# Kernel tuning notes

Measured on AMD Instinct MI355X. Metric: run time of the kernel, lower is better.

The kernel has to match this reference:

```python
import jax, jax.numpy as jnp
import numpy as np

HEAD_DIM = 128
N_HEADS = 32
N_KV_HEADS = 8
EPS = 1e-6
ROPE_THETA = 1e6
NEG_INF = -1e9


def _rms_norm(x, w):
    # per-head RMSNorm over last dim (head_dim), fp32 math like Qwen3RMSNorm
    xf = x.astype(jnp.float32)
    var = jnp.mean(xf * xf, axis=-1, keepdims=True)
    return (w * (xf * jax.lax.rsqrt(var + EPS))).astype(x.dtype)


def _rope_cos_sin(position_ids, dtype):
    # default rope: inv_freq = theta^(-2i/d), emb = cat(freqs, freqs)
    inv_freq = 1.0 / (ROPE_THETA ** (jnp.arange(0, HEAD_DIM, 2, dtype=jnp.float32) / HEAD_DIM))
    freqs = position_ids.astype(jnp.float32)[:, :, None] * inv_freq[None, None, :]  # [B,S,hd/2]
    emb = jnp.concatenate([freqs, freqs], axis=-1)  # [B,S,hd]
    return jnp.cos(emb).astype(dtype), jnp.sin(emb).astype(dtype)


def _rotate_half(x):
    x1, x2 = jnp.split(x, 2, axis=-1)
    return jnp.concatenate([-x2, x1], axis=-1)


def setup_inputs() -> dict:
    key = jax.random.key(0)
    ks = jax.random.split(key, 6)
    B, S, H = 1, 2048, 4096
    return {
        "hidden_states": jax.random.normal(ks[0], (B, S, H), jnp.float32),
        "position_ids": jnp.broadcast_to(jnp.arange(S, dtype=jnp.int32)[None, :], (B, S)),
        "Wq": jax.random.normal(ks[1], (N_HEADS * HEAD_DIM, H), jnp.float32) * 0.02,
        "Wk": jax.random.normal(ks[2], (N_KV_HEADS * HEAD_DIM, H), jnp.float32) * 0.02,
        "Wv": jax.random.normal(ks[3], (N_KV_HEADS * HEAD_DIM, H), jnp.float32) * 0.02,
        "Wo": jax.random.normal(ks[4], (H, N_HEADS * HEAD_DIM), jnp.float32) * 0.02,
        "q_norm_w": jnp.ones((HEAD_DIM,), jnp.float32),
        "k_norm_w": jnp.ones((HEAD_DIM,), jnp.float32),
    }


def reference(hidden_states, position_ids, Wq, Wk, Wv, Wo, q_norm_w, k_norm_w):
    B, S, H = hidden_states.shape
    scaling = HEAD_DIM ** -0.5
    n_rep = N_HEADS // N_KV_HEADS

    # projections (torch Linear: y = x @ W.T), reshape to [B, heads, S, hd]
    q = jnp.einsum('bsh,dh->bsd', hidden_states, Wq).reshape(B, S, N_HEADS, HEAD_DIM)
    k = jnp.einsum('bsh,dh->bsd', hidden_states, Wk).reshape(B, S, N_KV_HEADS, HEAD_DIM)
    v = jnp.einsum('bsh,dh->bsd', hidden_states, Wv).reshape(B, S, N_KV_HEADS, HEAD_DIM)

    q = _rms_norm(q, q_norm_w).transpose(0, 2, 1, 3)  # [B,nH,S,hd]
    k = _rms_norm(k, k_norm_w).transpose(0, 2, 1, 3)  # [B,nKV,S,hd]
    v = v.transpose(0, 2, 1, 3)

    cos, sin = _rope_cos_sin(position_ids, hidden_states.dtype)
    cos = cos[:, None, :, :]  # unsqueeze head dim
    sin = sin[:, None, :, :]
    q = q * cos + _rotate_half(q) * sin
    k = k * cos + _rotate_half(k) * sin

    # GQA repeat_kv
    k = jnp.repeat(k, n_rep, axis=1)
    v = jnp.repeat(v, n_rep, axis=1)

    scores = jnp.einsum('bhqd,bhkd->bhqk', q, k) * scaling
    causal = jnp.where(
        jnp.arange(S)[:, None] >= jnp.arange(S)[None, :], 0.0, NEG_INF
    ).astype(scores.dtype)
    scores = scores + causal[None, None, :, :]
    attn = jax.nn.softmax(scores.astype(jnp.float32), axis=-1).astype(q.dtype)

    out = jnp.einsum('bhqk,bhkd->bhqd', attn, v)
    out = out.transpose(0, 2, 1, 3).reshape(B, S, N_HEADS * HEAD_DIM)
    return jnp.einsum('bsd,hd->bsh', out, Wo)
```

## Files before the change

kernel.cpp:

```cpp
#include <hip/hip_runtime.h>
#include <hip/hip_bf16.h>

typedef unsigned short u16;
typedef __bf16 bf16x8 __attribute__((ext_vector_type(8)));
typedef u16 u16x4 __attribute__((ext_vector_type(4)));
typedef u16 u16x8 __attribute__((ext_vector_type(8)));
typedef float f32x4 __attribute__((ext_vector_type(4)));

#define S_LEN  2048
#define HID    4096
#define NHEADS 32
#define NKV    8
#define HD     128
#define QDIM   (NHEADS*HD)
#define KVDIM  (NKV*HD)
#define NT     (S_LEN/64)

__device__ __forceinline__ u16 f2bf(float f) {
  unsigned u = __float_as_uint(f);
  u += 0x7fff + ((u >> 16) & 1);
  return (u16)(u >> 16);
}
__device__ __forceinline__ void lds_load16(const u16* g, u16* l) {
  __builtin_amdgcn_global_load_lds(
      (__attribute__((address_space(1))) void*)(g),
      (__attribute__((address_space(3))) void*)(l), 16, 0, 0);
}

__global__ __launch_bounds__(256) void f2b4(
    const float* __restrict__ s0, u16* __restrict__ d0, long n0,
    const float* __restrict__ s1, u16* __restrict__ d1, long n1,
    const float* __restrict__ s2, u16* __restrict__ d2, long n2,
    const float* __restrict__ s3, u16* __restrict__ d3, long n3)
{
  const float* s; u16* d; long n; int b0, nb;
  const int b = blockIdx.x;
  if (b < 1024)      { s=s0; d=d0; n=n0; b0=0;    nb=1024; }
  else if (b < 3072) { s=s1; d=d1; n=n1; b0=1024; nb=2048; }
  else if (b < 3584) { s=s2; d=d2; n=n2; b0=3072; nb=512;  }
  else               { s=s3; d=d3; n=n3; b0=3584; nb=512;  }
  long i = (long)(b - b0)*256 + threadIdx.x;
  const long stride = (long)nb*256;
  for (; i < n; i += stride) {
    f32x4 a = ((const f32x4*)s)[i*2];
    f32x4 c = ((const f32x4*)s)[i*2 + 1];
    u16x8 o;
    #pragma unroll
    for (int j = 0; j < 4; ++j) { o[j] = f2bf(a[j]); o[4+j] = f2bf(c[j]); }
    ((u16x8*)d)[i] = o;
  }
}

__global__ __launch_bounds__(256) void f2b(
    const float* __restrict__ in, u16* __restrict__ out, long n8)
{
  long i = (long)blockIdx.x * blockDim.x + threadIdx.x;
  const long stride = (long)gridDim.x * blockDim.x;
  for (; i < n8; i += stride) {
    f32x4 a = ((const f32x4*)in)[i*2];
    f32x4 b = ((const f32x4*)in)[i*2 + 1];
    u16x8 o;
    #pragma unroll
    for (int j = 0; j < 4; ++j) { o[j] = f2bf(a[j]); o[4+j] = f2bf(b[j]); }
    ((u16x8*)out)[i] = o;
  }
}

template<int CMODE>
__global__ __launch_bounds__(512, 2) void gemm8(
    const u16* __restrict__ A, const u16* __restrict__ B,
    void* __restrict__ Cq, void* __restrict__ Ck, void* __restrict__ Cv,
    int M, int N, int K)
{
  __shared__ u16 lds[65536];
  const int tid  = threadIdx.x;
  const int lane = tid & 63;
  const int w    = tid >> 6;
  const int wr   = w >> 2, wc = w & 3;
  const int l16  = lane & 15, lhi = lane >> 4;
  const long arow0 = (long)blockIdx.y * 256;
  const long brow0 = (long)blockIdx.x * 256;
  const int ntiles = K >> 6;

  const u16* Ag[2]; const u16* Bg[2];
  #pragma unroll
  for (int r = 0; r < 2; ++r) {
    const int p  = r*4096 + w*512 + lane*8;
    const int lr = p >> 6;
    const int cu = (p & 63) ^ ((lr & 7) << 3);
    Ag[r] = A + (arow0 + (lr >> 6)*128 + (lr & 63))*(long)K + cu;
    Bg[r] = B + (brow0 + (lr >> 5)*64  + (lr & 31))*(long)K + cu;
  }
  u16* const dstA = lds + w*512;
  u16* const dstB = lds + 32768 + w*512;

  auto stageA = [&](int s, int kt) {
    const long so = (long)(kt*64) + (long)(s*64)*K;
    u16* d = dstA + (((kt & 1)*2 + s) << 13);
    lds_load16(Ag[0] + so, d);
    lds_load16(Ag[1] + so, d + 4096);
  };
  auto stageB = [&](int s, int kt) {
    const long so = (long)(kt*64) + (long)(s*32)*K;
    u16* d = dstB + (((kt & 1)*2 + s) << 13);
    lds_load16(Bg[0] + so, d);
    lds_load16(Bg[1] + so, d + 4096);
  };

  const int xr = (l16 & 7) << 3;
  int offA[4][2], offB[2][2];
  #pragma unroll
  for (int m2 = 0; m2 < 4; ++m2)
    #pragma unroll
    for (int ks = 0; ks < 2; ++ks)
      offA[m2][ks] = (wr*64 + m2*16 + l16)*64 + ((ks*32 + lhi*8) ^ xr);
  #pragma unroll
  for (int n2 = 0; n2 < 2; ++n2)
    #pragma unroll
    for (int ks = 0; ks < 2; ++ks)
      offB[n2][ks] = (wc*32 + n2*16 + l16)*64 + ((ks*32 + lhi*8) ^ xr);

  f32x4 acc[8][4] = {};

  stageA(0, 0); stageB(0, 0); stageB(1, 0); stageA(1, 0);
  stageA(0, 1); stageB(0, 1); stageB(1, 1);
  asm volatile("s_waitcnt vmcnt(6)" ::: "memory");
  __builtin_amdgcn_s_barrier();

  #pragma unroll 2
  for (int t = 0; t < ntiles; ++t) {
    const int Ab = (t & 1) << 14;
    const int Bb = 32768 + ((t & 1) << 14);
    bf16x8 af[4][2], bf[2][2], af2[4][2], bf2[2][2];

    #pragma unroll
    for (int m2 = 0; m2 < 4; ++m2)
      #pragma unroll
      for (int ks = 0; ks < 2; ++ks)
        af[m2][ks] = *(const bf16x8*)(lds + Ab + offA[m2][ks]);
    #pragma unroll
    for (int n2 = 0; n2 < 2; ++n2)
      #pragma unroll
      for (int ks = 0; ks < 2; ++ks)
        bf[n2][ks] = *(const bf16x8*)(lds + Bb + offB[n2][ks]);
    if (t + 1 < ntiles) stageA(1, t + 1);
    __builtin_amdgcn_s_barrier();
    asm volatile("s_waitcnt lgkmcnt(0)" ::: "memory");
    __builtin_amdgcn_s_setprio(1);
    #pragma unroll
    for (int m2 = 0; m2 < 4; ++m2)
      #pragma unroll
      for (int n2 = 0; n2 < 2; ++n2)
        #pragma unroll
        for (int ks = 0; ks < 2; ++ks)
          acc[m2][n2] = __builtin_amdgcn_mfma_f32_16x16x32_bf16(
              af[m2][ks], bf[n2][ks], acc[m2][n2], 0, 0, 0);
    __builtin_amdgcn_s_setprio(0);
    __builtin_amdgcn_s_barrier();

    #pragma unroll
    for (int n2 = 0; n2 < 2; ++n2)
      #pragma unroll
      for (int ks = 0; ks < 2; ++ks)
        bf2[n2][ks] = *(const bf16x8*)(lds + Bb + 8192 + offB[n2][ks]);
    if (t + 2 < ntiles) stageA(0, t + 2);
    __builtin_amdgcn_s_barrier();
    asm volatile("s_waitcnt lgkmcnt(0)" ::: "memory");
    __builtin_amdgcn_s_setprio(1);
    #pragma unroll
    for (int m2 = 0; m2 < 4; ++m2)
      #pragma unroll
      for (int n2 = 0; n2 < 2; ++n2)
        #pragma unroll
        for (int ks = 0; ks < 2; ++ks)
          acc[m2][2+n2] = __builtin_amdgcn_mfma_f32_16x16x32_bf16(
              af[m2][ks], bf2[n2][ks], acc[m2][2+n2], 0, 0, 0);
    __builtin_amdgcn_s_setprio(0);
    __builtin_amdgcn_s_barrier();

    #pragma unroll
    for (int m2 = 0; m2 < 4; ++m2)
      #pragma unroll
      for (int ks = 0; ks < 2; ++ks)
        af2[m2][ks] = *(const bf16x8*)(lds + Ab + 8192 + offA[m2][ks]);
    if (t + 2 < ntiles) stageB(0, t + 2);
    __builtin_amdgcn_s_barrier();
    asm volatile("s_waitcnt lgkmcnt(0)" ::: "memory");
    __builtin_amdgcn_s_setprio(1);
    #pragma unroll
    for (int m2 = 0; m2 < 4; ++m2)
      #pragma unroll
      for (int n2 = 0; n2 < 2; ++n2)
        #pragma unroll
        for (int ks = 0; ks < 2; ++ks)
          acc[4+m2][2+n2] = __builtin_amdgcn_mfma_f32_16x16x32_bf16(
              af2[m2][ks], bf2[n2][ks], acc[4+m2][2+n2], 0, 0, 0);
    __builtin_amdgcn_s_setprio(0);
    __builtin_amdgcn_s_barrier();

    if (t + 2 < ntiles) stageB(1, t + 2);
    __builtin_amdgcn_s_barrier();
    __builtin_amdgcn_s_setprio(1);
    #pragma unroll
    for (int m2 = 0; m2 < 4; ++m2)
      #pragma unroll
      for (int n2 = 0; n2 < 2; ++n2)
        #pragma unroll
        for (int ks = 0; ks < 2; ++ks)
          acc[4+m2][n2] = __builtin_amdgcn_mfma_f32_16x16x32_bf16(
              af2[m2][ks], bf[n2][ks], acc[4+m2][n2], 0, 0, 0);
    __builtin_amdgcn_s_setprio(0);
    if (t + 2 < ntiles) { asm volatile("s_waitcnt vmcnt(6)" ::: "memory"); }
    else                { asm volatile("s_waitcnt vmcnt(0)" ::: "memory"); }
    __builtin_amdgcn_s_barrier();
  }

  #pragma unroll
  for (int m = 0; m < 8; ++m) {
    const long row = arow0 + wr*128 + m*16 + lhi*4;
    #pragma unroll
    for (int n = 0; n < 4; ++n) {
      const long col = brow0 + wc*64 + n*16 + l16;
      if (CMODE == 1) {
        #pragma unroll
        for (int r = 0; r < 4; ++r)
          ((float*)Cq)[(row + r)*N + col] = acc[m][n][r];
      } else {
        if (blockIdx.x < 16) {
          #pragma unroll
          for (int r = 0; r < 4; ++r)
            ((u16*)Cq)[(row + r)*QDIM + col] = f2bf(acc[m][n][r]);
        } else if (blockIdx.x < 20) {
          #pragma unroll
          for (int r = 0; r < 4; ++r)
            ((u16*)Ck)[(row + r)*KVDIM + (col - QDIM)] = f2bf(acc[m][n][r]);
        } else {
          u16x4 o;
          #pragma unroll
          for (int r = 0; r < 4; ++r) o[r] = f2bf(acc[m][n][r]);
          *(u16x4*)((u16*)Cv + (col - QDIM - KVDIM)*(long)S_LEN + row) = o;
        }
      }
    }
  }
}

__global__ __launch_bounds__(512, 2) void gemmF(
    const u16* __restrict__ A, const u16* __restrict__ B,
    float* __restrict__ C, int M, int N, int K)
{
  __shared__ u16 lds[49152];
  const int tid  = threadIdx.x;
  const int lane = tid & 63;
  const int w    = tid >> 6;
  const int wr   = w >> 2, wc = w & 3;
  const int l16  = lane & 15, lhi = lane >> 4;
  const long arow0 = (long)blockIdx.y * 128;
  const long brow0 = (long)blockIdx.x * 256;
  const int ntiles = K >> 6;

  const int cu = ((lane & 7) ^ (lane >> 3)) * 8;
  const int rA  = (w >> 2)*64 + (w & 3)*8;
  const int rB1c = 128 + (w >> 2)*64 + (w & 3)*8;
  const u16* srcA  = A + (arow0 + rA   + (lane >> 3))*(long)K + cu;
  const u16* srcB0 = B + (brow0 + rA   + (lane >> 3))*(long)K + cu;
  const u16* srcB1 = B + (brow0 + rB1c + (lane >> 3))*(long)K + cu;
  u16* const dA  = lds + rA*64;
  u16* const dB0 = lds + 16384 + rA*64;
  u16* const dB1 = lds + 16384 + rB1c*64;

  auto stageA = [&](int s, int kt) {
    lds_load16(srcA + (long)(s*32)*K + kt*64,
               dA + ((kt & 1) << 13) + s*2048);
  };
  auto stageB = [&](int s, int kt) {
    const long so = (long)(s*32)*K + kt*64;
    const int  d  = ((kt & 1) << 14) + s*2048;
    lds_load16(srcB0 + so, dB0 + d);
    lds_load16(srcB1 + so, dB1 + d);
  };

  const int xr = (l16 & 7) << 3;
  int offA[2][2], offB[2][2];
  #pragma unroll
  for (int m = 0; m < 2; ++m)
    #pragma unroll
    for (int ks = 0; ks < 2; ++ks)
      offA[m][ks] = (wr*64 + m*16 + l16)*64 + ((ks*32 + lhi*8) ^ xr);
  #pragma unroll
  for (int n = 0; n < 2; ++n)
    #pragma unroll
    for (int ks = 0; ks < 2; ++ks)
      offB[n][ks] = (wc*64 + n*16 + l16)*64 + ((ks*32 + lhi*8) ^ xr);

  f32x4 acc[4][4] = {};

  stageA(0, 0); stageA(1, 0); stageB(0, 0); stageB(1, 0);
  if (ntiles > 1) { stageA(0, 1); stageB(0, 1); stageB(1, 1); }
  asm volatile("s_waitcnt vmcnt(5)" ::: "memory");
  __builtin_amdgcn_s_barrier();

  #pragma unroll 2
  for (int t = 0; t < ntiles; ++t) {
    const int Ab = (t & 1) << 13;
    const int Bb = 16384 + ((t & 1) << 14);
    bf16x8 af[2][2], bf[2][2], af2[2][2], bf2[2][2];

    #pragma unroll
    for (int m = 0; m < 2; ++m)
      #pragma unroll
      for (int ks = 0; ks < 2; ++ks)
        af[m][ks] = *(const bf16x8*)(lds + Ab + offA[m][ks]);
    #pragma unroll
    for (int n = 0; n < 2; ++n)
      #pragma unroll
      for (int ks = 0; ks < 2; ++ks)
        bf[n][ks] = *(const bf16x8*)(lds + Bb + offB[n][ks]);
    if (t + 1 < ntiles) stageA(1, t + 1);
    __builtin_amdgcn_s_barrier();
    asm volatile("s_waitcnt lgkmcnt(0)" ::: "memory");
    __builtin_amdgcn_s_setprio(1);
    #pragma unroll
    for (int m = 0; m < 2; ++m)
      #pragma unroll
      for (int n = 0; n < 2; ++n)
        #pragma unroll
        for (int ks = 0; ks < 2; ++ks)
          acc[m][n] = __builtin_amdgcn_mfma_f32_16x16x32_bf16(
              af[m][ks], bf[n][ks], acc[m][n], 0, 0, 0);
    __builtin_amdgcn_s_setprio(0);
    __builtin_amdgcn_s_barrier();

    #pragma unroll
    for (int n = 0; n < 2; ++n)
      #pragma unroll
      for (int ks = 0; ks < 2; ++ks)
        bf2[n][ks] = *(const bf16x8*)(lds + Bb + 2048 + offB[n][ks]);
    if (t + 2 < ntiles) stageA(0, t + 2);
    __builtin_amdgcn_s_barrier();
    asm volatile("s_waitcnt lgkmcnt(0)" ::: "memory");
    __builtin_amdgcn_s_setprio(1);
    #pragma unroll
    for (int m = 0; m < 2; ++m)
      #pragma unroll
      for (int n = 0; n < 2; ++n)
        #pragma unroll
        for (int ks = 0; ks < 2; ++ks)
          acc[m][2+n] = __builtin_amdgcn_mfma_f32_16x16x32_bf16(
              af[m][ks], bf2[n][ks], acc[m][2+n], 0, 0, 0);
    __builtin_amdgcn_s_setprio(0);
    __builtin_amdgcn_s_barrier();

    #pragma unroll
    for (int m = 0; m < 2; ++m)
      #pragma unroll
      for (int ks = 0; ks < 2; ++ks)
        af2[m][ks] = *(const bf16x8*)(lds + Ab + 2048 + offA[m][ks]);
    if (t + 2 < ntiles) stageB(0, t + 2);
    __builtin_amdgcn_s_barrier();
    asm volatile("s_waitcnt lgkmcnt(0)" ::: "memory");
    __builtin_amdgcn_s_setprio(1);
    #pragma unroll
    for (int m = 0; m < 2; ++m)
      #pragma unroll
      for (int n = 0; n < 2; ++n)
        #pragma unroll
        for (int ks = 0; ks < 2; ++ks)
          acc[2+m][2+n] = __builtin_amdgcn_mfma_f32_16x16x32_bf16(
              af2[m][ks], bf2[n][ks], acc[2+m][2+n], 0, 0, 0);
    __builtin_amdgcn_s_setprio(0);
    __builtin_amdgcn_s_barrier();

    if (t + 2 < ntiles) stageB(1, t + 2);
    __builtin_amdgcn_s_barrier();
    __builtin_amdgcn_s_setprio(1);
    #pragma unroll
    for (int m = 0; m < 2; ++m)
      #pragma unroll
      for (int n = 0; n < 2; ++n)
        #pragma unroll
        for (int ks = 0; ks < 2; ++ks)
          acc[2+m][n] = __builtin_amdgcn_mfma_f32_16x16x32_bf16(
              af2[m][ks], bf[n][ks], acc[2+m][n], 0, 0, 0);
    __builtin_amdgcn_s_setprio(0);
    if (t + 2 < ntiles) { asm volatile("s_waitcnt vmcnt(5)" ::: "memory"); }
    else                { asm volatile("s_waitcnt vmcnt(0)" ::: "memory"); }
    __builtin_amdgcn_s_barrier();
  }

  #pragma unroll
  for (int mi = 0; mi < 4; ++mi) {
    const long row = arow0 + wr*64 + (mi >> 1)*32 + (mi & 1)*16 + lhi*4;
    #pragma unroll
    for (int ni = 0; ni < 4; ++ni) {
      const long col = brow0 + wc*64 + (ni >> 1)*32 + (ni & 1)*16 + l16;
      #pragma unroll
      for (int r = 0; r < 4; ++r)
        C[(row + r)*N + col] = acc[mi][ni][r];
    }
  }
}

__global__ __launch_bounds__(256) void norm_rope2(
    u16* __restrict__ Qb, u16* __restrict__ Kb,
    const float* __restrict__ qw, const float* __restrict__ kw,
    const int* __restrict__ pos)
{
  const int row  = blockIdx.x * 4 + (threadIdx.x >> 6);
  const int lane = threadIdx.x & 63;
  u16* p; const float* nw; float sc; int s;
  if (row < S_LEN*NHEADS) {
    p = Qb + (long)row * HD; nw = qw; sc = 0.08838834764831845f; s = row >> 5;
  } else {
    const int r2 = row - S_LEN*NHEADS;
    p = Kb + (long)r2 * HD; nw = kw; sc = 1.0f; s = r2 >> 3;
  }

  float x1 = __uint_as_float(((unsigned)p[lane]) << 16);
  float x2 = __uint_as_float(((unsigned)p[lane + 64]) << 16);
  float ss = x1*x1 + x2*x2;
  #pragma unroll
  for (int m = 32; m >= 1; m >>= 1) ss += __shfl_xor(ss, m);
  const float inv = rsqrtf(ss * (1.0f/128.0f) + 1e-6f);
  x1 *= inv * nw[lane];
  x2 *= inv * nw[lane + 64];

  const float inv_freq = expf(-(float)lane * (13.815510557964274f / 64.0f));
  const float ang = (float)pos[s] * inv_freq;
  float sn, cs;
  sincosf(ang, &sn, &cs);
  p[lane]      = f2bf((x1*cs - x2*sn) * sc);
  p[lane + 64] = f2bf((x2*cs + x1*sn) * sc);
}

__global__ __launch_bounds__(256, 2) void attn(
    const u16* __restrict__ Q, const u16* __restrict__ K,
    const u16* __restrict__ VT, u16* __restrict__ O)
{
  __shared__ u16 Ks[2][64*128];
  __shared__ u16 Vt[2][128*64];
  __shared__ u16 Ps[4*16*64];

  const int tid  = threadIdx.x;
  const int lane = tid & 63;
  const int w    = tid >> 6;
  const int l16  = lane & 15, lhi = lane >> 4;
  const int h    = blockIdx.y;
  const int kh   = h >> 2;
  const int T    = (NT - 1) - ((blockIdx.x + blockIdx.y) & (NT - 1));
  const int qrow0 = T*64 + w*16;

  bf16x8 qf[4];
  #pragma unroll
  for (int ks = 0; ks < 4; ++ks)
    qf[ks] = *(const bf16x8*)(Q + (long)(qrow0 + l16)*QDIM + h*HD + ks*32 + lhi*8);

  auto stageK = [&](int buf, int t) {
    const long kv0 = t * 64;
    #pragma unroll
    for (int i = 0; i < 4; ++i) {
      const int r = w*16 + i*4 + lhi;
      lds_load16(K + (kv0 + r)*(long)KVDIM + kh*HD + ((l16*8) ^ ((r & 7) << 3)),
                 &Ks[buf][(w*16 + i*4)*128]);
    }
  };
  auto stageV = [&](int buf, int t) {
    const long kv0 = t * 64;
    #pragma unroll
    for (int i = 0; i < 4; ++i) {
      const int r = w*32 + i*8 + (lane >> 3);
      lds_load16(VT + (long)(kh*HD + r)*S_LEN + kv0 + (((lane & 7)*8) ^ ((r & 7) << 3)),
                 &Vt[buf][(w*32 + i*8)*64]);
    }
  };

  float mr[4] = {-1e30f,-1e30f,-1e30f,-1e30f};
  float lr[4] = {0.f,0.f,0.f,0.f};
  f32x4 of[8] = {};
  u16* Pw = Ps + w*16*64;

  stageK(0, 0); stageV(0, 0);

  for (int t = 0; t <= T; ++t) {
    const int cur = t & 1;
    const int kv0 = t * 64;
    const u16* Kc = Ks[cur];
    const u16* Vc = Vt[cur];

    asm volatile("s_waitcnt vmcnt(4)" ::: "memory");
    __builtin_amdgcn_s_barrier();

    f32x4 sa[4] = {};
    __builtin_amdgcn_s_setprio(1);
    #pragma unroll
    for (int n = 0; n < 4; ++n)
      #pragma unroll
      for (int ks = 0; ks < 4; ++ks) {
        bf16x8 kf = *(const bf16x8*)(
            Kc + (n*16 + l16)*128 + ((ks*32 + lhi*8) ^ ((l16 & 7) << 3)));
        sa[n] = __builtin_amdgcn_mfma_f32_16x16x32_bf16(qf[ks], kf, sa[n], 0, 0, 0);
      }
    __builtin_amdgcn_s_setprio(0);
    if (t < T) stageK(cur ^ 1, t + 1);

    const bool diag = (t == T);
    float pm[4];
    #pragma unroll
    for (int r = 0; r < 4; ++r) {
      const int grow = qrow0 + lhi*4 + r;
      #pragma unroll
      for (int n = 0; n < 4; ++n) {
        float sv = sa[n][r];
        if (diag && (kv0 + n*16 + l16 > grow)) sv = -1e9f;
        sa[n][r] = sv;
      }
      float p01 = fmaxf(sa[0][r], sa[1][r]);
      float p23 = fmaxf(sa[2][r], sa[3][r]);
      float pmx = fmaxf(p01, p23);
      pmx = fmaxf(pmx, __shfl_xor(pmx, 1));
      pmx = fmaxf(pmx, __shfl_xor(pmx, 2));
      pmx = fmaxf(pmx, __shfl_xor(pmx, 4));
      pmx = fmaxf(pmx, __shfl_xor(pmx, 8));
      pm[r] = pmx;
    }
    bool need = (pm[0] > mr[0] + 8.f) | (pm[1] > mr[1] + 8.f) |
                (pm[2] > mr[2] + 8.f) | (pm[3] > mr[3] + 8.f);
    if (__any(need)) {
      #pragma unroll
      for (int r = 0; r < 4; ++r) {
        const float mnew  = fmaxf(mr[r], pm[r]);
        const float alpha = __expf(mr[r] - mnew);
        mr[r] = mnew;
        lr[r] *= alpha;
        #pragma unroll
        for (int c = 0; c < 8; ++c) of[c][r] *= alpha;
      }
    }
    #pragma unroll
    for (int r = 0; r < 4; ++r) {
      float rsum = 0.f;
      #pragma unroll
      for (int n = 0; n < 4; ++n) {
        float pv = __expf(sa[n][r] - mr[r]);
        sa[n][r] = pv;
        rsum += pv;
      }
      rsum += __shfl_xor(rsum, 1);
      rsum += __shfl_xor(rsum, 2);
      rsum += __shfl_xor(rsum, 4);
      rsum += __shfl_xor(rsum, 8);
      lr[r] += rsum;
    }

    #pragma unroll
    for (int r = 0; r < 4; ++r) {
      const int prow = lhi*4 + r;
      #pragma unroll
      for (int n = 0; n < 4; ++n)
        Pw[prow*64 + ((n*16 + l16) ^ ((prow & 7) << 3))] = f2bf(sa[n][r]);
    }

    if (t < T) { asm volatile("s_waitcnt vmcnt(4)" ::: "memory"); }
    else       { asm volatile("s_waitcnt vmcnt(0)" ::: "memory"); }
    __builtin_amdgcn_s_barrier();

    __builtin_amdgcn_s_setprio(1);
    #pragma unroll
    for (int ks = 0; ks < 2; ++ks) {
      bf16x8 pf = *(const bf16x8*)(
          Pw + l16*64 + ((ks*32 + lhi*8) ^ ((l16 & 7) << 3)));
      #pragma unroll
      for (int c = 0; c < 8; ++c) {
        bf16x8 vf = *(const bf16x8*)(
            Vc + (c*16 + l16)*64 + ((ks*32 + lhi*8) ^ ((l16 & 7) << 3)));
        of[c] = __builtin_amdgcn_mfma_f32_16x16x32_bf16(pf, vf, of[c], 0, 0, 0);
      }
    }
    __builtin_amdgcn_s_setprio(0);
    if (t < T) stageV(cur ^ 1, t + 1);
  }

  #pragma unroll
  for (int r = 0; r < 4; ++r) {
    const float invl = 1.0f / lr[r];
    const long orow = (long)(qrow0 + lhi*4 + r) * QDIM + h*HD;
    #pragma unroll
    for (int c = 0; c < 8; ++c)
      O[orow + c*16 + l16] = f2bf(of[c][r] * invl);
  }
}

extern "C" void kernel_launch(void* const* d_in, const int* in_sizes, int n_in,
                              void* d_out, int out_size, void* d_ws, size_t ws_size,
                              hipStream_t stream) {
  (void)in_sizes; (void)n_in; (void)out_size; (void)ws_size;
  const float* hs  = (const float*)d_in[0];
  const int*   pos = (const int*)d_in[1];
  const float* Wq  = (const float*)d_in[2];
  const float* Wk  = (const float*)d_in[3];
  const float* Wv  = (const float*)d_in[4];
  const float* Wo  = (const float*)d_in[5];
  const float* qw  = (const float*)d_in[6];
  const float* kw  = (const float*)d_in[7];

  u16* hsB = (u16*)d_ws;
  u16* W1  = hsB + (long)S_LEN*HID;
  u16* WkB = W1  + (long)QDIM*HID;
  u16* WvB = WkB + (long)KVDIM*HID;
  u16* Kb  = WvB + (long)KVDIM*HID;
  u16* VT  = Kb  + (long)S_LEN*KVDIM;
  u16* AO  = VT  + (long)KVDIM*S_LEN;
  u16* Qb  = (u16*)d_out;

  f2b4<<<4096, 256, 0, stream>>>(hs, hsB, (long)S_LEN*HID/8,
                                 Wq, W1,  (long)QDIM*HID/8,
                                 Wk, WkB, (long)KVDIM*HID/8,
                                 Wv, WvB, (long)KVDIM*HID/8);

  gemm8<3><<<dim3((QDIM+2*KVDIM)/256, S_LEN/256), 512, 0, stream>>>(
      hsB, W1, Qb, Kb, VT, S_LEN, QDIM+2*KVDIM, HID);

  norm_rope2<<<(S_LEN*NHEADS + S_LEN*NKV)/4, 256, 0, stream>>>(
      Qb, Kb, qw, kw, pos);

  f2b<<<2048, 256, 0, stream>>>(Wo, W1, (long)HID*QDIM/8);

  attn<<<dim3(NT, NHEADS), 256, 0, stream>>>(Qb, Kb, VT, AO);

  gemmF<<<dim3(HID/256, S_LEN/128), 512, 0, stream>>>(
      AO, W1, (float*)d_out, S_LEN, HID, QDIM);
}
```

Baseline: 399.3 us.

## Use 128-row query tiles with 32x32 MFMA in attention, single-buffered KV

The attention kernel now gives each block 128 query rows (32 per wave) and uses 32x32x16 bf16 MFMA in place of 16x16x32. Each K/V tile loaded into LDS is therefore reused by twice as many query rows, and the grid is halved. The double-buffered async prefetch is replaced by single buffers with a __syncthreads before and after each tile, so global loads no longer overlap compute. Register pressure also rises from the 16-row softmax state and the f32x16 accumulators, which may lower occupancy.

Measured after the change: 445.4 us. 11.5% more time.

```diff
diff --git a/kernel.cpp b/kernel.cpp
--- a/kernel.cpp
+++ b/kernel.cpp
@@ -6,6 +6,7 @@
 typedef u16 u16x4 __attribute__((ext_vector_type(4)));
 typedef u16 u16x8 __attribute__((ext_vector_type(8)));
 typedef float f32x4 __attribute__((ext_vector_type(4)));
+typedef float f32x16 __attribute__((ext_vector_type(16)));
 
 #define S_LEN  2048
 #define HID    4096
@@ -14,7 +15,6 @@
 #define HD     128
 #define QDIM   (NHEADS*HD)
 #define KVDIM  (NKV*HD)
-#define NT     (S_LEN/64)
 
 __device__ __forceinline__ u16 f2bf(float f) {
   unsigned u = __float_as_uint(f);
@@ -437,156 +437,152 @@
     const u16* __restrict__ Q, const u16* __restrict__ K,
     const u16* __restrict__ VT, u16* __restrict__ O)
 {
-  __shared__ u16 Ks[2][64*128];
-  __shared__ u16 Vt[2][128*64];
-  __shared__ u16 Ps[4*16*64];
+  __shared__ u16 Ks[64*128];
+  __shared__ u16 Vt[128*64];
+  __shared__ u16 Ps[4][32*64];
 
   const int tid  = threadIdx.x;
   const int lane = tid & 63;
   const int w    = tid >> 6;
   const int l16  = lane & 15, lhi = lane >> 4;
+  const int l32  = lane & 31, lh  = lane >> 5;
   const int h    = blockIdx.y;
   const int kh   = h >> 2;
-  const int T    = (NT - 1) - ((blockIdx.x + blockIdx.y) & (NT - 1));
-  const int qrow0 = T*64 + w*16;
-
-  bf16x8 qf[4];
-  #pragma unroll
-  for (int ks = 0; ks < 4; ++ks)
-    qf[ks] = *(const bf16x8*)(Q + (long)(qrow0 + l16)*QDIM + h*HD + ks*32 + lhi*8);
-
-  auto stageK = [&](int buf, int t) {
-    const long kv0 = t * 64;
+  const int Tq   = 15 - ((blockIdx.x + blockIdx.y) & 15);
+  const int qrow0 = Tq*128 + w*32;
+  const int ntile = 2*Tq + 2;
+
+  bf16x8 qf[8];
+  #pragma unroll
+  for (int s = 0; s < 8; ++s)
+    qf[s] = *(const bf16x8*)(Q + (long)(qrow0 + l32)*QDIM + h*HD + s*16 + lh*8);
+
+  float mr[16], lr[16];
+  #pragma unroll
+  for (int r = 0; r < 16; ++r) { mr[r] = -1e30f; lr[r] = 0.f; }
+  f32x16 of[4] = {};
+  u16* Pw = Ps[w];
+
+  for (int t = 0; t < ntile; ++t) {
+    const int kv0 = t * 64;
     #pragma unroll
     for (int i = 0; i < 4; ++i) {
-      const int r = w*16 + i*4 + lhi;
-      lds_load16(K + (kv0 + r)*(long)KVDIM + kh*HD + ((l16*8) ^ ((r & 7) << 3)),
-                 &Ks[buf][(w*16 + i*4)*128]);
+      const int r   = w*16 + i*4 + lhi;
+      const int col = (l16*8) ^ ((r & 7) << 3);
+      lds_load16(K + (long)(kv0 + r)*KVDIM + kh*HD + col,
+                 Ks + (w*16 + i*4)*128);
     }
-  };
-  auto stageV = [&](int buf, int t) {
-    const long kv0 = t * 64;
     #pragma unroll
     for (int i = 0; i < 4; ++i) {
-      const int r = w*32 + i*8 + (lane >> 3);
-      lds_load16(VT + (long)(kh*HD + r)*S_LEN + kv0 + (((lane & 7)*8) ^ ((r & 7) << 3)),
-                 &Vt[buf][(w*32 + i*8)*64]);
+      const int r   = w*32 + i*8 + (lane >> 3);
+      const int col = ((lane & 7)*8) ^ ((r & 7) << 3);
+      lds_load16(VT + (long)(kh*HD + r)*S_LEN + kv0 + col,
+                 Vt + (w*32 + i*8)*64);
     }
-  };
-
-  float mr[4] = {-1e30f,-1e30f,-1e30f,-1e30f};
-  float lr[4] = {0.f,0.f,0.f,0.f};
-  f32x4 of[8] = {};
-  u16* Pw = Ps + w*16*64;
-
-  stageK(0, 0); stageV(0, 0);
-
-  for (int t = 0; t <= T; ++t) {
-    const int cur = t & 1;
-    const int kv0 = t * 64;
-    const u16* Kc = Ks[cur];
-    const u16* Vc = Vt[cur];
-
-    asm volatile("s_waitcnt vmcnt(4)" ::: "memory");
-    __builtin_amdgcn_s_barrier();
-
-    f32x4 sa[4] = {};
-    __builtin_amdgcn_s_setprio(1);
-    #pragma unroll
-    for (int n = 0; n < 4; ++n)
+    __syncthreads();
+
+    if (kv0 <= qrow0 + 31) {
+      f32x16 sa[2] = {};
+      __builtin_amdgcn_s_setprio(1);
+      #pragma unroll
+      for (int s = 0; s < 8; ++s) {
+        const int dco = (s*16 + lh*8);
+        #pragma unroll
+        for (int n = 0; n < 2; ++n) {
+          bf16x8 kf = *(const bf16x8*)(
+              Ks + (n*32 + l32)*128 + (dco ^ ((l32 & 7) << 3)));
+          sa[n] = __builtin_amdgcn_mfma_f32_32x32x16_bf16(
+              qf[s], kf, sa[n], 0, 0, 0);
+        }
+      }
+      __builtin_amdgcn_s_setprio(0);
+
+      const bool diag = (kv0 + 63 > qrow0);
+      if (diag) {
+        #pragma unroll
+        for (int n = 0; n < 2; ++n)
+          #pragma unroll
+          for (int r = 0; r < 16; ++r) {
+            const int q  = qrow0 + (r & 3) + 8*(r >> 2) + 4*lh;
+            const int kv = kv0 + n*32 + l32;
+            if (kv > q) sa[n][r] = -1e9f;
+          }
+      }
+
+      float mx[16];
+      #pragma unroll
+      for (int r = 0; r < 16; ++r) {
+        float m2 = fmaxf(sa[0][r], sa[1][r]);
+        m2 = fmaxf(m2, __shfl_xor(m2, 1));
+        m2 = fmaxf(m2, __shfl_xor(m2, 2));
+        m2 = fmaxf(m2, __shfl_xor(m2, 4));
+        m2 = fmaxf(m2, __shfl_xor(m2, 8));
+        m2 = fmaxf(m2, __shfl_xor(m2, 16));
+        mx[r] = m2;
+      }
+      bool need = false;
+      #pragma unroll
+      for (int r = 0; r < 16; ++r) need |= (mx[r] > mr[r] + 8.f);
+      if (__any(need)) {
+        #pragma unroll
+        for (int r = 0; r < 16; ++r) {
+          const float mnew  = fmaxf(mr[r], mx[r]);
+          const float alpha = __expf(mr[r] - mnew);
+          mr[r] = mnew;
+          lr[r] *= alpha;
+          #pragma unroll
+          for (int dt = 0; dt < 4; ++dt) of[dt][r] *= alpha;
+        }
+      }
+      #pragma unroll
+      for (int r = 0; r < 16; ++r) {
+        float p0 = __expf(sa[0][r] - mr[r]);
+        float p1 = __expf(sa[1][r] - mr[r]);
+        sa[0][r] = p0; sa[1][r] = p1;
+        float rs = p0 + p1;
+        rs += __shfl_xor(rs, 1);
+        rs += __shfl_xor(rs, 2);
+        rs += __shfl_xor(rs, 4);
+        rs += __shfl_xor(rs, 8);
+        rs += __shfl_xor(rs, 16);
+        lr[r] += rs;
+      }
+
+      #pragma unroll
+      for (int n = 0; n < 2; ++n)
+        #pragma unroll
+        for (int r = 0; r < 16; ++r) {
+          const int qr = (r & 3) + 8*(r >> 2) + 4*lh;
+          Pw[qr*64 + ((n*32 + l32) ^ ((qr & 7) << 3))] = f2bf(sa[n][r]);
+        }
+
+      __builtin_amdgcn_s_setprio(1);
       #pragma unroll
       for (int ks = 0; ks < 4; ++ks) {
-        bf16x8 kf = *(const bf16x8*)(
-            Kc + (n*16 + l16)*128 + ((ks*32 + lhi*8) ^ ((l16 & 7) << 3)));
-        sa[n] = __builtin_amdgcn_mfma_f32_16x16x32_bf16(qf[ks], kf, sa[n], 0, 0, 0);
+        const int kco = (ks*16 + lh*8);
+        bf16x8 pf = *(const bf16x8*)(
+            Pw + l32*64 + (kco ^ ((l32 & 7) << 3)));
+        #pragma unroll
+        for (int dt = 0; dt < 4; ++dt) {
+          bf16x8 vf = *(const bf16x8*)(
+              Vt + (dt*32 + l32)*64 + (kco ^ ((l32 & 7) << 3)));
+          of[dt] = __builtin_amdgcn_mfma_f32_32x32x16_bf16(
+              pf, vf, of[dt], 0, 0, 0);
+        }
       }
-    __builtin_amdgcn_s_setprio(0);
-    if (t < T) stageK(cur ^ 1, t + 1);
-
-    const bool diag = (t == T);
-    float pm[4];
-    #pragma unroll
-    for (int r = 0; r < 4; ++r) {
-      const int grow = qrow0 + lhi*4 + r;
-      #pragma unroll
-      for (int n = 0; n < 4; ++n) {
-        float sv = sa[n][r];
-        if (diag && (kv0 + n*16 + l16 > grow)) sv = -1e9f;
-        sa[n][r] = sv;
-      }
-      float p01 = fmaxf(sa[0][r], sa[1][r]);
-      float p23 = fmaxf(sa[2][r], sa[3][r]);
-      float pmx = fmaxf(p01, p23);
-      pmx = fmaxf(pmx, __shfl_xor(pmx, 1));
-      pmx = fmaxf(pmx, __shfl_xor(pmx, 2));
-      pmx = fmaxf(pmx, __shfl_xor(pmx, 4));
-      pmx = fmaxf(pmx, __shfl_xor(pmx, 8));
-      pm[r] = pmx;
+      __builtin_amdgcn_s_setprio(0);
     }
-    bool need = (pm[0] > mr[0] + 8.f) | (pm[1] > mr[1] + 8.f) |
-                (pm[2] > mr[2] + 8.f) | (pm[3] > mr[3] + 8.f);
-    if (__any(need)) {
-      #pragma unroll
-      for (int r = 0; r < 4; ++r) {
-        const float mnew  = fmaxf(mr[r], pm[r]);
-        const float alpha = __expf(mr[r] - mnew);
-        mr[r] = mnew;
-        lr[r] *= alpha;
-        #pragma unroll
-        for (int c = 0; c < 8; ++c) of[c][r] *= alpha;
-      }
-    }
-    #pragma unroll
-    for (int r = 0; r < 4; ++r) {
-      float rsum = 0.f;
-      #pragma unroll
-      for (int n = 0; n < 4; ++n) {
-        float pv = __expf(sa[n][r] - mr[r]);
-        sa[n][r] = pv;
-        rsum += pv;
-      }
-      rsum += __shfl_xor(rsum, 1);
-      rsum += __shfl_xor(rsum, 2);
-      rsum += __shfl_xor(rsum, 4);
-      rsum += __shfl_xor(rsum, 8);
-      lr[r] += rsum;
-    }
-
-    #pragma unroll
-    for (int r = 0; r < 4; ++r) {
-      const int prow = lhi*4 + r;
-      #pragma unroll
-      for (int n = 0; n < 4; ++n)
-        Pw[prow*64 + ((n*16 + l16) ^ ((prow & 7) << 3))] = f2bf(sa[n][r]);
-    }
-
-    if (t < T) { asm volatile("s_waitcnt vmcnt(4)" ::: "memory"); }
-    else       { asm volatile("s_waitcnt vmcnt(0)" ::: "memory"); }
-    __builtin_amdgcn_s_barrier();
-
-    __builtin_amdgcn_s_setprio(1);
-    #pragma unroll
-    for (int ks = 0; ks < 2; ++ks) {
-      bf16x8 pf = *(const bf16x8*)(
-          Pw + l16*64 + ((ks*32 + lhi*8) ^ ((l16 & 7) << 3)));
-      #pragma unroll
-      for (int c = 0; c < 8; ++c) {
-        bf16x8 vf = *(const bf16x8*)(
-            Vc + (c*16 + l16)*64 + ((ks*32 + lhi*8) ^ ((l16 & 7) << 3)));
-        of[c] = __builtin_amdgcn_mfma_f32_16x16x32_bf16(pf, vf, of[c], 0, 0, 0);
-      }
-    }
-    __builtin_amdgcn_s_setprio(0);
-    if (t < T) stageV(cur ^ 1, t + 1);
-  }
-
-  #pragma unroll
-  for (int r = 0; r < 4; ++r) {
+    __syncthreads();
+  }
+
+  #pragma unroll
+  for (int r = 0; r < 16; ++r) {
+    const int qr = (r & 3) + 8*(r >> 2) + 4*lh;
     const float invl = 1.0f / lr[r];
-    const long orow = (long)(qrow0 + lhi*4 + r) * QDIM + h*HD;
-    #pragma unroll
-    for (int c = 0; c < 8; ++c)
-      O[orow + c*16 + l16] = f2bf(of[c][r] * invl);
+    const long orow = (long)(qrow0 + qr)*QDIM + h*HD;
+    #pragma unroll
+    for (int dt = 0; dt < 4; ++dt)
+      O[orow + dt*32 + l32] = f2bf(of[dt][r] * invl);
   }
 }
 
@@ -625,7 +621,7 @@
 
   f2b<<<2048, 256, 0, stream>>>(Wo, W1, (long)HID*QDIM/8);
 
-  attn<<<dim3(NT, NHEADS), 256, 0, stream>>>(Qb, Kb, VT, AO);
+  attn<<<dim3(16, NHEADS), 256, 0, stream>>>(Qb, Kb, VT, AO);
 
   gemmF<<<dim3(HID/256, S_LEN/128), 512, 0, stream>>>(
       AO, W1, (float*)d_out, S_LEN, HID, QDIM);
```

## Read V directly from global, remap attention blocks across XCDs, raise occupancy

Applied to the files above, without the earlier changes.

The attention kernel stops staging V tiles in LDS and feeds the PV MFMAs straight from the transposed V in global memory, which halves the shared memory footprint. Launch bounds go from 2 to 4 blocks per CU. The grid is flattened and remapped so blocks sharing a head are grouped on the same XCD, aiming for better L2 reuse of K and V. Explicit vmcnt waits are replaced by full __syncthreads. In exchange, V loads are no longer prefetched, so global memory latency is exposed inside the MFMA loop, and there is more barrier overhead.

After: 511.6 us. 1.28x slower.

```diff
diff --git a/kernel.cpp b/kernel.cpp
--- a/kernel.cpp
+++ b/kernel.cpp
@@ -433,21 +433,23 @@
   p[lane + 64] = f2bf((x2*cs + x1*sn) * sc);
 }
 
-__global__ __launch_bounds__(256, 2) void attn(
+__global__ __launch_bounds__(256, 4) void attn(
     const u16* __restrict__ Q, const u16* __restrict__ K,
     const u16* __restrict__ VT, u16* __restrict__ O)
 {
   __shared__ u16 Ks[2][64*128];
-  __shared__ u16 Vt[2][128*64];
   __shared__ u16 Ps[4*16*64];
 
   const int tid  = threadIdx.x;
   const int lane = tid & 63;
   const int w    = tid >> 6;
   const int l16  = lane & 15, lhi = lane >> 4;
-  const int h    = blockIdx.y;
-  const int kh   = h >> 2;
-  const int T    = (NT - 1) - ((blockIdx.x + blockIdx.y) & (NT - 1));
+
+  const int lid = ((blockIdx.x & 7) << 7) + (blockIdx.x >> 3);
+  const int h   = lid >> 5;
+  const int xx  = lid & 31;
+  const int kh  = h >> 2;
+  const int T   = (NT - 1) - ((xx + h) & (NT - 1));
   const int qrow0 = T*64 + w*16;
 
   bf16x8 qf[4];
@@ -456,21 +458,12 @@
     qf[ks] = *(const bf16x8*)(Q + (long)(qrow0 + l16)*QDIM + h*HD + ks*32 + lhi*8);
 
   auto stageK = [&](int buf, int t) {
-    const long kv0 = t * 64;
     #pragma unroll
     for (int i = 0; i < 4; ++i) {
-      const int r = w*16 + i*4 + lhi;
-      lds_load16(K + (kv0 + r)*(long)KVDIM + kh*HD + ((l16*8) ^ ((r & 7) << 3)),
+      const int r   = w*16 + i*4 + lhi;
+      const int col = (l16*8) ^ ((r & 7) << 3);
+      lds_load16(K + (long)(t*64 + r)*KVDIM + kh*HD + col,
                  &Ks[buf][(w*16 + i*4)*128]);
-    }
-  };
-  auto stageV = [&](int buf, int t) {
-    const long kv0 = t * 64;
-    #pragma unroll
-    for (int i = 0; i < 4; ++i) {
-      const int r = w*32 + i*8 + (lane >> 3);
-      lds_load16(VT + (long)(kh*HD + r)*S_LEN + kv0 + (((lane & 7)*8) ^ ((r & 7) << 3)),
-                 &Vt[buf][(w*32 + i*8)*64]);
     }
   };
 
@@ -479,16 +472,13 @@
   f32x4 of[8] = {};
   u16* Pw = Ps + w*16*64;
 
-  stageK(0, 0); stageV(0, 0);
+  stageK(0, 0);
+  __syncthreads();
 
   for (int t = 0; t <= T; ++t) {
     const int cur = t & 1;
     const int kv0 = t * 64;
     const u16* Kc = Ks[cur];
-    const u16* Vc = Vt[cur];
-
-    asm volatile("s_waitcnt vmcnt(4)" ::: "memory");
-    __builtin_amdgcn_s_barrier();
 
     f32x4 sa[4] = {};
     __builtin_amdgcn_s_setprio(1);
@@ -501,6 +491,7 @@
         sa[n] = __builtin_amdgcn_mfma_f32_16x16x32_bf16(qf[ks], kf, sa[n], 0, 0, 0);
       }
     __builtin_amdgcn_s_setprio(0);
+
     if (t < T) stageK(cur ^ 1, t + 1);
 
     const bool diag = (t == T);
@@ -560,10 +551,6 @@
         Pw[prow*64 + ((n*16 + l16) ^ ((prow & 7) << 3))] = f2bf(sa[n][r]);
     }
 
-    if (t < T) { asm volatile("s_waitcnt vmcnt(4)" ::: "memory"); }
-    else       { asm volatile("s_waitcnt vmcnt(0)" ::: "memory"); }
-    __builtin_amdgcn_s_barrier();
-
     __builtin_amdgcn_s_setprio(1);
     #pragma unroll
     for (int ks = 0; ks < 2; ++ks) {
@@ -572,12 +559,13 @@
       #pragma unroll
       for (int c = 0; c < 8; ++c) {
         bf16x8 vf = *(const bf16x8*)(
-            Vc + (c*16 + l16)*64 + ((ks*32 + lhi*8) ^ ((l16 & 7) << 3)));
+            VT + (long)(kh*HD + c*16 + l16)*S_LEN + kv0 + ks*32 + lhi*8);
         of[c] = __builtin_amdgcn_mfma_f32_16x16x32_bf16(pf, vf, of[c], 0, 0, 0);
       }
     }
     __builtin_amdgcn_s_setprio(0);
-    if (t < T) stageV(cur ^ 1, t + 1);
+
+    __syncthreads();
   }
 
   #pragma unroll
@@ -625,7 +613,7 @@
 
   f2b<<<2048, 256, 0, stream>>>(Wo, W1, (long)HID*QDIM/8);
 
-  attn<<<dim3(NT, NHEADS), 256, 0, stream>>>(Qb, Kb, VT, AO);
+  attn<<<dim3(NT*NHEADS), 256, 0, stream>>>(Qb, Kb, VT, AO);
 
   gemmF<<<dim3(HID/256, S_LEN/128), 512, 0, stream>>>(
       AO, W1, (float*)d_out, S_LEN, HID, QDIM);
```
